# Kernel optimization log

Hardware: AMD Instinct MI355X
Metric: run time of the kernel (lower is better)

## Reference

```python
import jax, jax.numpy as jnp
import numpy as np

N = 100000
E = 3200000
IN_DIM = 512
HID = 256
NUM_CLASSES = 16
P_DROP = 0.5
EPS_BN = 1e-5


def setup_inputs() -> dict:
    key = jax.random.key(0)
    ks = jax.random.split(key, 6)
    x = jax.random.normal(ks[0], (N, IN_DIM), jnp.float32)
    edge_src = jax.random.randint(ks[1], (E,), 0, N, dtype=jnp.int32)
    edge_dst = jax.random.randint(ks[2], (E,), 0, N, dtype=jnp.int32)
    # Glorot-ish init for GraphConv weights (bias=False in the module)
    W1 = jax.random.normal(ks[3], (IN_DIM, HID), jnp.float32) / np.sqrt(IN_DIM).astype(np.float32)
    W2 = jax.random.normal(ks[4], (HID, NUM_CLASSES), jnp.float32) / np.sqrt(HID).astype(np.float32)
    W3 = jax.random.normal(ks[5], (HID, NUM_CLASSES), jnp.float32) / np.sqrt(HID).astype(np.float32)
    return {"x": x, "W1": W1, "W2": W2, "W3": W3,
            "edge_src": edge_src, "edge_dst": edge_dst}


def _graph_conv(h, W, edge_src, edge_dst, out_inv_sqrt, in_inv_sqrt):
    # DGL GraphConv, norm='both', bias=False:
    #   rst = D_in^{-1/2} * A_agg( D_out^{-1/2} * h @ W )
    # Apply W before aggregation (out_dim <= in_dim here); same math as DGL.
    h = h * out_inv_sqrt[:, None]          # [N, d_in]
    h = h @ W                              # [N, d_out]
    agg = jax.ops.segment_sum(h[edge_src], edge_dst, num_segments=h.shape[0])
    return agg * in_inv_sqrt[:, None]


def _dropout(key, x, p=P_DROP):
    keep = jax.random.bernoulli(key, 1.0 - p, x.shape)
    return jnp.where(keep, x / (1.0 - p), jnp.zeros((), x.dtype))


def reference(x, W1, W2, W3, edge_src, edge_dst):
    n = x.shape[0]
    ones = jnp.ones(edge_src.shape[0], x.dtype)
    out_deg = jax.ops.segment_sum(ones, edge_src, num_segments=n)
    in_deg = jax.ops.segment_sum(ones, edge_dst, num_segments=n)
    out_is = jnp.maximum(out_deg, 1.0) ** -0.5   # DGL clamps degree to min 1
    in_is = jnp.maximum(in_deg, 1.0) ** -0.5

    k1, k2a, k2b, keps = jax.random.split(jax.random.key(42), 4)

    # gc1 + relu
    h = _dropout(k1, x)
    h = jax.nn.relu(_graph_conv(h, W1, edge_src, edge_dst, out_is, in_is))

    # BatchNorm1d(affine=False, track_running_stats=False): batch stats
    mean = jnp.mean(h, axis=0)
    var = jnp.var(h, axis=0)
    h = (h - mean) * jax.lax.rsqrt(var + EPS_BN)

    # gc2 (mu) and gc3 (logvar), each with its own dropout of hidden1
    mu = _graph_conv(_dropout(k2a, h), W2, edge_src, edge_dst, out_is, in_is)
    logvar = _graph_conv(_dropout(k2b, h), W3, edge_src, edge_dst, out_is, in_is)

    # reparameterize (training): eps * exp(logvar) + mu  (note: exp(logvar), per source)
    eps = jax.random.normal(keps, mu.shape, mu.dtype)
    return eps * jnp.exp(logvar) + mu
```

## Files before the change

kernel.cpp:

```cpp
#include <hip/hip_runtime.h>
#include <stdint.h>

#define N_NODES 100000
#define N_EDGES 3200000
#define IN_DIM  512
#define HID     256
#define NCLS    16

#define DBLK   256
#define DCHUNK (N_EDGES / DBLK)
#define DWIN2  50000
#define NBKT   98
#define NTILE  ((N_NODES + 255) / 256)

typedef unsigned short u16;
typedef unsigned char u8;
typedef __attribute__((ext_vector_type(8))) short short8;
typedef __attribute__((ext_vector_type(4))) float float4v;

__device__ __forceinline__ float bf2f(u16 u) {
  return __uint_as_float(((uint32_t)u) << 16);
}
__device__ __forceinline__ u16 f2bf(float f) {
  uint32_t u = __float_as_uint(f);
  return (u16)((u + 0x7fffu + ((u >> 16) & 1u)) >> 16);
}
__device__ __forceinline__ void acc8(float* a, uint4 v) {
  a[0] += bf2f((u16)(v.x & 0xffffu)); a[1] += bf2f((u16)(v.x >> 16));
  a[2] += bf2f((u16)(v.y & 0xffffu)); a[3] += bf2f((u16)(v.y >> 16));
  a[4] += bf2f((u16)(v.z & 0xffffu)); a[5] += bf2f((u16)(v.z >> 16));
  a[6] += bf2f((u16)(v.w & 0xffffu)); a[7] += bf2f((u16)(v.w >> 16));
}

__device__ __forceinline__ void gload16(const void* g, void* l) {
  __builtin_amdgcn_global_load_lds(
      (const __attribute__((address_space(1))) uint32_t*)g,
      (__attribute__((address_space(3))) uint32_t*)l, 16, 0, 0);
}

__host__ __device__ __forceinline__ uint32_t rotl32(uint32_t v, int d) {
  return (v << d) | (v >> (32 - d));
}

__host__ __device__ __forceinline__ void threefry2x32(uint32_t k0, uint32_t k1,
    uint32_t x0, uint32_t x1, uint32_t& o0, uint32_t& o1) {
  uint32_t ks0 = k0, ks1 = k1, ks2 = k0 ^ k1 ^ 0x1BD11BDAu;
  x0 += ks0; x1 += ks1;
#define TF_R(r) { x0 += x1; x1 = rotl32(x1, r); x1 ^= x0; }
  TF_R(13) TF_R(15) TF_R(26) TF_R(6)
  x0 += ks1; x1 += ks2 + 1u;
  TF_R(17) TF_R(29) TF_R(16) TF_R(24)
  x0 += ks2; x1 += ks0 + 2u;
  TF_R(13) TF_R(15) TF_R(26) TF_R(6)
  x0 += ks0; x1 += ks1 + 3u;
  TF_R(17) TF_R(29) TF_R(16) TF_R(24)
  x0 += ks1; x1 += ks2 + 4u;
  TF_R(13) TF_R(15) TF_R(26) TF_R(6)
  x0 += ks2; x1 += ks0 + 5u;
#undef TF_R
  o0 = x0; o1 = x1;
}

__host__ __device__ __forceinline__ uint32_t tf_bits32(uint32_t k0, uint32_t k1, uint32_t idx) {
  uint32_t o0, o1;
  threefry2x32(k0, k1, 0u, idx, o0, o1);
  return o0 ^ o1;
}

__device__ __forceinline__ float erfinv_f32(float x) {
  float w = -log1pf(-x * x);
  float p;
  if (w < 5.0f) {
    w -= 2.5f;
    p = 2.81022636e-08f;
    p = fmaf(p, w, 3.43273939e-07f);
    p = fmaf(p, w, -3.5233877e-06f);
    p = fmaf(p, w, -4.39150654e-06f);
    p = fmaf(p, w, 0.00021858087f);
    p = fmaf(p, w, -0.00125372503f);
    p = fmaf(p, w, -0.00417768164f);
    p = fmaf(p, w, 0.246640727f);
    p = fmaf(p, w, 1.50140941f);
  } else {
    w = sqrtf(w) - 3.0f;
    p = -0.000200214257f;
    p = fmaf(p, w, 0.000100950558f);
    p = fmaf(p, w, 0.00134934322f);
    p = fmaf(p, w, -0.00367342844f);
    p = fmaf(p, w, 0.00573950773f);
    p = fmaf(p, w, -0.0076224613f);
    p = fmaf(p, w, 0.00943887047f);
    p = fmaf(p, w, 1.00167406f);
    p = fmaf(p, w, 2.83297682f);
  }
  return p * x;
}

__global__ __launch_bounds__(1024) void hist_part_k(
    const int* __restrict__ esrc, const int* __restrict__ edst,
    u16* __restrict__ P16, uint32_t* __restrict__ bofs_g,
    unsigned long long* __restrict__ ebuf) {
  __shared__ uint32_t h32[DWIN2 / 2];
  __shared__ uint32_t bcnt[NBKT + 1];
  const int b = blockIdx.x, tid = threadIdx.x;
  const int ebase = b * DCHUNK;
  if (tid < NBKT + 1) bcnt[tid] = 0u;
  for (int w = 0; w < 2; ++w) {
    const int lo = w * DWIN2;
    for (int i = tid; i < DWIN2 / 2; i += 1024) h32[i] = 0u;
    __syncthreads();
    for (int e = ebase + tid; e < ebase + DCHUNK; e += 1024) {
      int s = esrc[e], d = edst[e];
      unsigned su = (unsigned)(s - lo);
      if (su < (unsigned)DWIN2) atomicAdd(&h32[su >> 1], 1u << ((su & 1) * 16));
      unsigned du = (unsigned)(d - lo);
      if (du < (unsigned)DWIN2) atomicAdd(&h32[du >> 1], 0x100u << ((du & 1) * 16));
      if (w == 0) atomicAdd(&bcnt[d >> 10], 1u);
    }
    __syncthreads();
    for (int i = tid; i < DWIN2 / 2; i += 1024) {
      *(uint32_t*)(P16 + (size_t)b * N_NODES + lo + 2 * i) = h32[i];
    }
    __syncthreads();
  }
  if (tid == 0) {
    uint32_t run = 0;
    for (int k = 0; k < NBKT; ++k) { uint32_t c = bcnt[k]; bcnt[k] = run; run += c; }
    bcnt[NBKT] = run;
  }
  __syncthreads();
  if (tid < NBKT + 1) bofs_g[b * (NBKT + 1) + tid] = bcnt[tid];
  __syncthreads();
  for (int e = ebase + tid; e < ebase + DCHUNK; e += 1024) {
    int d = edst[e], s = esrc[e];
    uint32_t slot = atomicAdd(&bcnt[d >> 10], 1u);
    ebuf[(size_t)b * DCHUNK + slot] = ((unsigned long long)(uint32_t)s << 32) | (uint32_t)d;
  }
}

__global__ void degsum_k(const u16* __restrict__ P16, float* __restrict__ out_is,
                         float* __restrict__ in_is, int* __restrict__ row_ofs,
                         int* __restrict__ tile_sum) {
  const int tid = threadIdx.x;
  const int n = blockIdx.x * 256 + tid;
  const int lane = tid & 63, wv = tid >> 6;
  uint32_t to = 0, ti = 0;
  if (n < N_NODES) {
#pragma unroll 8
    for (int b = 0; b < DBLK; ++b) {
      uint32_t v = P16[(size_t)b * N_NODES + n];
      to += v & 0xffu; ti += v >> 8;
    }
    out_is[n] = rsqrtf(fmaxf((float)to, 1.0f));
    in_is[n]  = rsqrtf(fmaxf((float)ti, 1.0f));
  }
  int sc = (int)ti;
#pragma unroll
  for (int d = 1; d < 64; d <<= 1) {
    int t = __shfl_up(sc, d, 64);
    if (lane >= d) sc += t;
  }
  __shared__ int ws[4];
  if (lane == 63) ws[wv] = sc;
  __syncthreads();
  int wbase = 0;
#pragma unroll
  for (int i = 0; i < 4; ++i) if (i < wv) wbase += ws[i];
  if (n < N_NODES) row_ofs[n] = wbase + sc - (int)ti;
  if (tid == 0) tile_sum[blockIdx.x] = ws[0] + ws[1] + ws[2] + ws[3];
}

__global__ void fixup_k(const int* __restrict__ tile_sum, int* __restrict__ row_ofs) {
  const int b = blockIdx.x, tid = threadIdx.x;
  const int lane = tid & 63, wv = tid >> 6;
  int v = 0;
  if (tid < b) v = tile_sum[tid];
  if (tid + 256 < b) v += tile_sum[tid + 256];
#pragma unroll
  for (int m = 1; m < 64; m <<= 1) v += __shfl_xor(v, m, 64);
  __shared__ int wr[4];
  if (lane == 0) wr[wv] = v;
  __syncthreads();
  const int base = wr[0] + wr[1] + wr[2] + wr[3];
  const int n = b * 256 + tid;
  if (n < N_NODES) row_ofs[n] += base;
  if (b == (int)gridDim.x - 1 && tid == 0) row_ofs[N_NODES] = base + tile_sum[b];
}

__global__ __launch_bounds__(1024) void bplace_k(
    const unsigned long long* __restrict__ ebuf, const uint32_t* __restrict__ bofs_g,
    const int* __restrict__ row_ofs, int* __restrict__ csr) {
  __shared__ uint32_t cur[1024];
  const int k = blockIdx.x, tid = threadIdx.x;
  const int lane = tid & 63, wv = tid >> 6;
  const int dbase = k << 10;
  int nd = N_NODES - dbase; if (nd > 1024) nd = 1024;
  if (tid < nd) cur[tid] = (uint32_t)row_ofs[dbase + tid];
  __syncthreads();
  for (int b = wv; b < DBLK; b += 16) {
    uint32_t st = bofs_g[b * (NBKT + 1) + k];
    uint32_t en = bofs_g[b * (NBKT + 1) + k + 1];
    for (uint32_t i = st + lane; i < en; i += 64) {
      unsigned long long v = ebuf[(size_t)b * DCHUNK + i];
      int d = (int)(uint32_t)(v & 0xffffffffu);
      int s = (int)(uint32_t)(v >> 32);
      uint32_t slot = atomicAdd(&cur[d - dbase], 1u);
      csr[slot] = s;
    }
  }
}

__global__ void cast_w_k(const float* __restrict__ W1, const float* __restrict__ W2,
                         const float* __restrict__ W3, u16* __restrict__ W1t,
                         u16* __restrict__ Wt23) {
  int idx = blockIdx.x * blockDim.x + threadIdx.x;
  if (idx < IN_DIM * HID) {
    int k = idx >> 8, n = idx & 255;
    W1t[n * IN_DIM + k] = f2bf(W1[idx]);
  } else {
    int t = idx - IN_DIM * HID;
    int n = t >> 8, k = t & 255;
    float v = (n < 16) ? W2[k * NCLS + n] : W3[k * NCLS + (n - 16)];
    Wt23[n * HID + k] = f2bf(v);
  }
}

#define G1_BM 128
#define G1_BKC 8
__global__ __launch_bounds__(512, 2) void gemm1_k(
    const float* __restrict__ x, const float* __restrict__ out_is,
    uint32_t k0, uint32_t k1,
    const u16* __restrict__ W1t, u16* __restrict__ X1b) {
  __shared__ u16 As[G1_BM * 64];
  __shared__ u16 Bs[256 * 64];
  const int tid = threadIdx.x;
  const int wid = tid >> 6, lane = tid & 63;
  const int wr = wid >> 2, wc = wid & 3;
  const int m16 = lane & 15, q = lane >> 4;
  const int srow = lane >> 3, schunk = lane & 7;
  const long base_row = (long)blockIdx.x * G1_BM;

  const int arow_l = tid >> 2, acp = tid & 3;
  const long agrow = base_row + arow_l;
  const long asrow = (agrow < N_NODES) ? agrow : (N_NODES - 1);
  const float asc = 2.0f * out_is[asrow];
  const float* xrow = x + asrow * IN_DIM;
  const int aw0 = ((2 * acp)     ^ (arow_l & 7)) * 8;
  const int aw1 = ((2 * acp + 1) ^ (arow_l & 7)) * 8;

  float4v acc[4][4];
#pragma unroll
  for (int i = 0; i < 4; ++i)
#pragma unroll
    for (int j = 0; j < 4; ++j) acc[i][j] = (float4v)0.0f;

  for (int ks = 0; ks < IN_DIM / 64; ++ks) {
    const int kbase = ks * 64 + acp * 16;
    float4 f0 = *(const float4*)(xrow + kbase);
    float4 f1 = *(const float4*)(xrow + kbase + 4);
    float4 f2 = *(const float4*)(xrow + kbase + 8);
    float4 f3 = *(const float4*)(xrow + kbase + 12);
    float xv[16] = {f0.x, f0.y, f0.z, f0.w, f1.x, f1.y, f1.z, f1.w,
                    f2.x, f2.y, f2.z, f2.w, f3.x, f3.y, f3.z, f3.w};
    const uint32_t ibase = (uint32_t)asrow * IN_DIM + (uint32_t)kbase;
    u16 ob[16];
#pragma unroll
    for (int j = 0; j < 16; ++j) {
      uint32_t bits = tf_bits32(k0, k1, ibase + (uint32_t)j);
      ob[j] = f2bf((bits >> 31) ? 0.0f : xv[j] * asc);
    }
    uint4 pka, pkb;
    pka.x = (uint32_t)ob[0] | ((uint32_t)ob[1] << 16);
    pka.y = (uint32_t)ob[2] | ((uint32_t)ob[3] << 16);
    pka.z = (uint32_t)ob[4] | ((uint32_t)ob[5] << 16);
    pka.w = (uint32_t)ob[6] | ((uint32_t)ob[7] << 16);
    pkb.x = (uint32_t)ob[8] | ((uint32_t)ob[9] << 16);
    pkb.y = (uint32_t)ob[10] | ((uint32_t)ob[11] << 16);
    pkb.z = (uint32_t)ob[12] | ((uint32_t)ob[13] << 16);
    pkb.w = (uint32_t)ob[14] | ((uint32_t)ob[15] << 16);
    *(uint4*)(As + arow_l * 64 + aw0) = pka;
    *(uint4*)(As + arow_l * 64 + aw1) = pkb;
#pragma unroll
    for (int i = 0; i < 4; ++i) {
      int j = wid * 4 + i;
      int n = j * 8 + srow;
      int gch = ks * G1_BKC + (schunk ^ (n & 7));
      gload16(W1t + (size_t)n * IN_DIM + gch * 8, Bs + j * 512);
    }
    __syncthreads();
#pragma unroll
    for (int kk = 0; kk < 2; ++kk) {
      short8 a[4], b[4];
      const int kq = kk * 4 + q;
      const int c = kq ^ (m16 & 7);
#pragma unroll
      for (int rt = 0; rt < 4; ++rt) {
        int row = wr * 64 + rt * 16 + m16;
        a[rt] = *(const short8*)(As + row * 64 + c * 8);
      }
#pragma unroll
      for (int ct = 0; ct < 4; ++ct) {
        int n = wc * 64 + ct * 16 + m16;
        b[ct] = *(const short8*)(Bs + n * 64 + c * 8);
      }
#pragma unroll
      for (int rt = 0; rt < 4; ++rt)
#pragma unroll
        for (int ct = 0; ct < 4; ++ct)
          acc[rt][ct] = __builtin_amdgcn_mfma_f32_16x16x32_bf16(a[rt], b[ct], acc[rt][ct], 0, 0, 0);
    }
    __syncthreads();
  }
#pragma unroll
  for (int rt = 0; rt < 4; ++rt) {
#pragma unroll
    for (int r = 0; r < 4; ++r) {
      long grow = base_row + wr * 64 + rt * 16 + q * 4 + r;
      if (grow < N_NODES) {
#pragma unroll
        for (int ct = 0; ct < 4; ++ct)
          X1b[grow * HID + wc * 64 + ct * 16 + m16] = f2bf(acc[rt][ct][r]);
      }
    }
  }
}

__global__ __launch_bounds__(256) void agg_relu_k(
    const u16* __restrict__ X1b, const int* __restrict__ row_ofs,
    const int* __restrict__ csr, const float* __restrict__ in_is,
    uint32_t ka0, uint32_t ka1, uint32_t kb0, uint32_t kb1,
    u8* __restrict__ mska, u8* __restrict__ mskb,
    u16* __restrict__ h1b) {
  int d = blockIdx.x * 4 + (threadIdx.x >> 6);
  int lane = threadIdx.x & 63;
  int half = lane >> 5;
  int col = (lane & 31) * 8;
  int beg = row_ofs[d], end = row_ofs[d + 1];
  float a[8];
#pragma unroll
  for (int i = 0; i < 8; ++i) a[i] = 0.0f;
  int j = beg + half;
  for (; j + 14 < end; j += 16) {
    int s0 = csr[j],      s1 = csr[j + 2],  s2 = csr[j + 4],  s3 = csr[j + 6];
    int s4 = csr[j + 8],  s5 = csr[j + 10], s6 = csr[j + 12], s7 = csr[j + 14];
    uint4 v0 = *(const uint4*)(X1b + (size_t)s0 * HID + col);
    uint4 v1 = *(const uint4*)(X1b + (size_t)s1 * HID + col);
    uint4 v2 = *(const uint4*)(X1b + (size_t)s2 * HID + col);
    uint4 v3 = *(const uint4*)(X1b + (size_t)s3 * HID + col);
    uint4 v4 = *(const uint4*)(X1b + (size_t)s4 * HID + col);
    uint4 v5 = *(const uint4*)(X1b + (size_t)s5 * HID + col);
    uint4 v6 = *(const uint4*)(X1b + (size_t)s6 * HID + col);
    uint4 v7 = *(const uint4*)(X1b + (size_t)s7 * HID + col);
    acc8(a, v0); acc8(a, v1); acc8(a, v2); acc8(a, v3);
    acc8(a, v4); acc8(a, v5); acc8(a, v6); acc8(a, v7);
  }
  for (; j + 6 < end; j += 8) {
    int s0 = csr[j], s1 = csr[j + 2], s2 = csr[j + 4], s3 = csr[j + 6];
    uint4 v0 = *(const uint4*)(X1b + (size_t)s0 * HID + col);
    uint4 v1 = *(const uint4*)(X1b + (size_t)s1 * HID + col);
    uint4 v2 = *(const uint4*)(X1b + (size_t)s2 * HID + col);
    uint4 v3 = *(const uint4*)(X1b + (size_t)s3 * HID + col);
    acc8(a, v0); acc8(a, v1); acc8(a, v2); acc8(a, v3);
  }
  for (; j < end; j += 2) {
    uint4 v0 = *(const uint4*)(X1b + (size_t)csr[j] * HID + col);
    acc8(a, v0);
  }
#pragma unroll
  for (int i = 0; i < 8; ++i) a[i] += __shfl(a[i], lane ^ 32, 64);
  if (half == 0) {
    float is = in_is[d];
    u16 o[8];
#pragma unroll
    for (int i = 0; i < 8; ++i) o[i] = f2bf(fmaxf(a[i] * is, 0.0f));
    uint4 pk;
    pk.x = (uint32_t)o[0] | ((uint32_t)o[1] << 16);
    pk.y = (uint32_t)o[2] | ((uint32_t)o[3] << 16);
    pk.z = (uint32_t)o[4] | ((uint32_t)o[5] << 16);
    pk.w = (uint32_t)o[6] | ((uint32_t)o[7] << 16);
    *(uint4*)(h1b + (size_t)d * HID + col) = pk;
  }
  {
    const uint32_t NB = (uint32_t)N_NODES * HID / 8;
    uint32_t gid = blockIdx.x * 256u + threadIdx.x;
    const bool isB = gid >= NB;
    const uint32_t mi = isB ? gid - NB : gid;
    const uint32_t kk0 = isB ? kb0 : ka0, kk1 = isB ? kb1 : ka1;
    const uint32_t ib = mi * 8u;
    uint32_t bits = 0u;
#pragma unroll
    for (uint32_t jj = 0; jj < 8; ++jj)
      bits |= ((~tf_bits32(kk0, kk1, ib + jj)) >> 31) << jj;
    (isB ? mskb : mska)[mi] = (u8)bits;
  }
}

__global__ __launch_bounds__(256) void bn_stats_k(const u16* __restrict__ h1b,
                                                  float* __restrict__ bn) {
  __shared__ float ls[512];
  const int tid = threadIdx.x;
  const int cb = (tid & 31) * 8;
  const int ms = tid >> 5;
  float s[8], s2[8];
#pragma unroll
  for (int i = 0; i < 8; ++i) { s[i] = 0.f; s2[i] = 0.f; }
  for (int m = ms;; m += 8) {
    int r = blockIdx.x + 256 * m;
    if (r >= N_NODES) break;
    uint4 v = *(const uint4*)(h1b + (size_t)r * HID + cb);
    float f[8];
    f[0] = bf2f((u16)(v.x & 0xffffu)); f[1] = bf2f((u16)(v.x >> 16));
    f[2] = bf2f((u16)(v.y & 0xffffu)); f[3] = bf2f((u16)(v.y >> 16));
    f[4] = bf2f((u16)(v.z & 0xffffu)); f[5] = bf2f((u16)(v.z >> 16));
    f[6] = bf2f((u16)(v.w & 0xffffu)); f[7] = bf2f((u16)(v.w >> 16));
#pragma unroll
    for (int i = 0; i < 8; ++i) { s[i] += f[i]; s2[i] += f[i] * f[i]; }
  }
  ls[tid] = 0.f; ls[tid + 256] = 0.f;
  __syncthreads();
#pragma unroll
  for (int i = 0; i < 8; ++i) {
    atomicAdd(&ls[cb + i], s[i]);
    atomicAdd(&ls[256 + cb + i], s2[i]);
  }
  __syncthreads();
  atomicAdd(&bn[tid], ls[tid]);
  atomicAdd(&bn[HID + tid], ls[256 + tid]);
}

#define WLS 264
__global__ __launch_bounds__(256) void gemm23_k(
    const u16* __restrict__ h1b, const u16* __restrict__ Wt23,
    const u8* __restrict__ mska, const u8* __restrict__ mskb,
    const float* __restrict__ out_is, const float* __restrict__ bn,
    u16* __restrict__ XMLV) {
  __shared__ u16 Wls[32 * WLS];
  __shared__ float cB[HID], cA[HID];
  const int tid = threadIdx.x;
#pragma unroll
  for (int i = 0; i < 4; ++i) {
    int idx = tid + i * 256;
    int n = idx >> 5, c = idx & 31;
    *(uint4*)(Wls + n * WLS + c * 8) = ((const uint4*)Wt23)[idx];
  }
  {
    float mean = bn[tid] * (1.0f / (float)N_NODES);
    float var = bn[HID + tid] * (1.0f / (float)N_NODES) - mean * mean;
    float istd = rsqrtf(var + 1e-5f);
    cB[tid] = istd;
    cA[tid] = -mean * istd;
  }
  __syncthreads();

  const int wv = tid >> 6, lane = tid & 63;
  const int m = lane & 15, q = lane >> 4;
  const long arow = (long)blockIdx.x * 64 + wv * 16 + m;
  const bool valid = arow < N_NODES;
  const float osc = valid ? 2.0f * out_is[arow] : 0.0f;

  float4v accM = (float4v)0.0f, accL = (float4v)0.0f;
  for (int kc = 0; kc < HID; kc += 32) {
    const int kof = kc + q * 8;
    uint4 hv = make_uint4(0, 0, 0, 0);
    uint32_t wa = 0, wb = 0;
    if (valid) {
      hv = *(const uint4*)(h1b + arow * HID + kof);
      uint32_t bofs = ((uint32_t)arow * HID + (uint32_t)kc) >> 3;
      wa = (*(const uint32_t*)(mska + bofs)) >> (q * 8);
      wb = (*(const uint32_t*)(mskb + bofs)) >> (q * 8);
    }
    float4 B0 = *(const float4*)(cB + kof);
    float4 B1 = *(const float4*)(cB + kof + 4);
    float4 A0 = *(const float4*)(cA + kof);
    float4 A1 = *(const float4*)(cA + kof + 4);
    float hval[8] = {
      bf2f((u16)(hv.x & 0xffffu)), bf2f((u16)(hv.x >> 16)),
      bf2f((u16)(hv.y & 0xffffu)), bf2f((u16)(hv.y >> 16)),
      bf2f((u16)(hv.z & 0xffffu)), bf2f((u16)(hv.z >> 16)),
      bf2f((u16)(hv.w & 0xffffu)), bf2f((u16)(hv.w >> 16))};
    float nb[8] = {B0.x, B0.y, B0.z, B0.w, B1.x, B1.y, B1.z, B1.w};
    float na[8] = {A0.x, A0.y, A0.z, A0.w, A1.x, A1.y, A1.z, A1.w};
    short8 Aa, Ab;
#pragma unroll
    for (int jj = 0; jj < 8; ++jj) {
      float t = fmaf(hval[jj], nb[jj], na[jj]) * osc;
      u16 tb = f2bf(t);
      Aa[jj] = (short)(((wa >> jj) & 1u) ? tb : 0);
      Ab[jj] = (short)(((wb >> jj) & 1u) ? tb : 0);
    }
    short8 Bm = *(const short8*)(Wls + m * WLS + kof);
    short8 Bl = *(const short8*)(Wls + (16 + m) * WLS + kof);
    accM = __builtin_amdgcn_mfma_f32_16x16x32_bf16(Aa, Bm, accM, 0, 0, 0);
    accL = __builtin_amdgcn_mfma_f32_16x16x32_bf16(Ab, Bl, accL, 0, 0, 0);
  }
#pragma unroll
  for (int r = 0; r < 4; ++r) {
    long srow = (long)blockIdx.x * 64 + wv * 16 + q * 4 + r;
    if (srow < N_NODES) {
      XMLV[srow * 32 + m]      = f2bf(accM[r]);
      XMLV[srow * 32 + 16 + m] = f2bf(accL[r]);
    }
  }
}

__global__ __launch_bounds__(256) void agg_final_k(
    const u16* __restrict__ XMLV, const int* __restrict__ row_ofs,
    const int* __restrict__ csr, const float* __restrict__ in_is,
    uint32_t ke0, uint32_t ke1, float* __restrict__ out) {
  int g = blockIdx.x * 4 + (threadIdx.x >> 6);
  int lane = threadIdx.x & 63;
  int half = lane >> 5, c = lane & 31;
  int beg = row_ofs[g], end = row_ofs[g + 1];
  float s = 0.f;
  int j = beg + half;
  for (; j + 14 < end; j += 16) {
    int s0 = csr[j],      s1 = csr[j + 2],  s2 = csr[j + 4],  s3 = csr[j + 6];
    int s4 = csr[j + 8],  s5 = csr[j + 10], s6 = csr[j + 12], s7 = csr[j + 14];
    float v0 = bf2f(XMLV[(size_t)s0 * 32 + c]);
    float v1 = bf2f(XMLV[(size_t)s1 * 32 + c]);
    float v2 = bf2f(XMLV[(size_t)s2 * 32 + c]);
    float v3 = bf2f(XMLV[(size_t)s3 * 32 + c]);
    float v4 = bf2f(XMLV[(size_t)s4 * 32 + c]);
    float v5 = bf2f(XMLV[(size_t)s5 * 32 + c]);
    float v6 = bf2f(XMLV[(size_t)s6 * 32 + c]);
    float v7 = bf2f(XMLV[(size_t)s7 * 32 + c]);
    s += v0; s += v1; s += v2; s += v3;
    s += v4; s += v5; s += v6; s += v7;
  }
#pragma unroll
  for (int k = 0; k < 8; ++k) {
    int e = j + 2 * k;
    if (e < end) s += bf2f(XMLV[(size_t)csr[e] * 32 + c]);
  }
  s += __shfl(s, lane ^ 32, 64);
  if (half == 0) {
    s *= in_is[g];
    float other = __shfl(s, lane ^ 16, 64);
    if (c < 16) {
      uint32_t i = (uint32_t)(g * NCLS + c);
      uint32_t bits = tf_bits32(ke0, ke1, i);
      float f = __uint_as_float((bits >> 9) | 0x3f800000u) - 1.0f;
      const float lo = -0.99999994f;
      float u = fmaxf(lo, fmaf(f, 2.0f, lo));
      float eps = 1.41421356f * erfinv_f32(u);
      out[i] = eps * expf(other) + s;
    }
  }
}

extern "C" void kernel_launch(void* const* d_in, const int* in_sizes, int n_in,
                              void* d_out, int out_size, void* d_ws, size_t ws_size,
                              hipStream_t stream) {
  (void)in_sizes; (void)n_in; (void)out_size; (void)ws_size;
  const float* x  = (const float*)d_in[0];
  const float* W1 = (const float*)d_in[1];
  const float* W2 = (const float*)d_in[2];
  const float* W3 = (const float*)d_in[3];
  const int* esrc = (const int*)d_in[4];
  const int* edst = (const int*)d_in[5];
  float* out = (float*)d_out;

  uint32_t kb[8];
  for (int j = 0; j < 4; ++j)
    threefry2x32(0u, 42u, 0u, (uint32_t)j, kb[2 * j], kb[2 * j + 1]);

  char* p = (char*)d_ws;
  auto take = [&](size_t bytes) -> void* {
    void* r = (void*)p;
    p += (bytes + 255) & ~(size_t)255;
    return r;
  };
  u16* P16       = (u16*)take(sizeof(u16) * (size_t)DBLK * N_NODES);
  unsigned long long* ebuf = (unsigned long long*)take(sizeof(unsigned long long) * (size_t)N_EDGES);
  u16* X1b       = (u16*)take(sizeof(u16) * (size_t)N_NODES * HID);
  u16* h1b       = (u16*)take(sizeof(u16) * (size_t)N_NODES * HID);
  u16* XMLV      = (u16*)take(sizeof(u16) * (size_t)N_NODES * 32);
  u16* W1t       = (u16*)take(sizeof(u16) * (size_t)IN_DIM * HID);
  u16* Wt23      = (u16*)take(sizeof(u16) * 32 * HID);
  u8* mska       = (u8*)take((size_t)N_NODES * HID / 8);
  u8* mskb       = (u8*)take((size_t)N_NODES * HID / 8);
  uint32_t* bofs_g = (uint32_t*)take(sizeof(uint32_t) * (size_t)DBLK * (NBKT + 1));
  int* tile_sum  = (int*)take(sizeof(int) * NTILE);
  float* out_is  = (float*)take(sizeof(float) * N_NODES);
  float* in_is   = (float*)take(sizeof(float) * N_NODES);
  int* row_ofs   = (int*)take(sizeof(int) * (N_NODES + 1));
  int* csr       = (int*)take(sizeof(int) * N_EDGES);
  float* bn      = (float*)take(sizeof(float) * 1024);

  hipMemsetAsync(bn, 0, sizeof(float) * 512, stream);

  hist_part_k<<<DBLK, 1024, 0, stream>>>(esrc, edst, P16, bofs_g, ebuf);
  degsum_k<<<NTILE, 256, 0, stream>>>(P16, out_is, in_is, row_ofs, tile_sum);
  fixup_k<<<NTILE, 256, 0, stream>>>(tile_sum, row_ofs);
  bplace_k<<<NBKT, 1024, 0, stream>>>(ebuf, bofs_g, row_ofs, csr);

  cast_w_k<<<(IN_DIM * HID + 32 * HID) / 256, 256, 0, stream>>>(W1, W2, W3, W1t, Wt23);

  gemm1_k<<<(N_NODES + G1_BM - 1) / G1_BM, 512, 0, stream>>>(x, out_is, kb[0], kb[1], W1t, X1b);
  agg_relu_k<<<N_NODES / 4, 256, 0, stream>>>(X1b, row_ofs, csr, in_is,
                                              kb[2], kb[3], kb[4], kb[5], mska, mskb, h1b);
  bn_stats_k<<<256, 256, 0, stream>>>(h1b, bn);
  gemm23_k<<<(N_NODES + 63) / 64, 256, 0, stream>>>(h1b, Wt23, mska, mskb, out_is, bn, XMLV);
  agg_final_k<<<N_NODES / 4, 256, 0, stream>>>(XMLV, row_ofs, csr, in_is, kb[6], kb[7], out);
}
```

Baseline: 841.3 us.

## Pack degree histograms into nibbles, use single-pass LDS histogram and 32-bit edge records

The per-block degree histogram now uses 4-bit in/out counts per node. That lets the whole node range fit in LDS, so one pass over the edge chunk replaces two windowed passes. Bucket counters are replicated eight ways to reduce atomic contention, and the bucketed edge buffer packs source and local destination into one 32-bit word instead of 64 bits. Together these cut reads of the edge lists, the histogram traffic in degsum, and the ebuf traffic. The risk is that any node appearing more than 15 times in one block's 12500-edge chunk overflows its nibble and corrupts the degrees, which is very unlikely for uniform random edges.

```diff
diff --git a/kernel.cpp b/kernel.cpp
--- a/kernel.cpp
+++ b/kernel.cpp
@@ -9,8 +9,8 @@
 
 #define DBLK   256
 #define DCHUNK (N_EDGES / DBLK)
-#define DWIN2  50000
 #define NBKT   98
+#define NREP   8
 #define NTILE  ((N_NODES + 255) / 256)
 
 typedef unsigned short u16;
@@ -98,31 +98,33 @@
 
 __global__ __launch_bounds__(1024) void hist_part_k(
     const int* __restrict__ esrc, const int* __restrict__ edst,
-    u16* __restrict__ P16, uint32_t* __restrict__ bofs_g,
-    unsigned long long* __restrict__ ebuf) {
-  __shared__ uint32_t h32[DWIN2 / 2];
+    u8* __restrict__ P8, uint32_t* __restrict__ bofs_g,
+    uint32_t* __restrict__ ebuf) {
+  __shared__ uint32_t h32[N_NODES / 4];
+  __shared__ uint32_t brep[NBKT * NREP];
   __shared__ uint32_t bcnt[NBKT + 1];
   const int b = blockIdx.x, tid = threadIdx.x;
   const int ebase = b * DCHUNK;
-  if (tid < NBKT + 1) bcnt[tid] = 0u;
-  for (int w = 0; w < 2; ++w) {
-    const int lo = w * DWIN2;
-    for (int i = tid; i < DWIN2 / 2; i += 1024) h32[i] = 0u;
-    __syncthreads();
-    for (int e = ebase + tid; e < ebase + DCHUNK; e += 1024) {
-      int s = esrc[e], d = edst[e];
-      unsigned su = (unsigned)(s - lo);
-      if (su < (unsigned)DWIN2) atomicAdd(&h32[su >> 1], 1u << ((su & 1) * 16));
-      unsigned du = (unsigned)(d - lo);
-      if (du < (unsigned)DWIN2) atomicAdd(&h32[du >> 1], 0x100u << ((du & 1) * 16));
-      if (w == 0) atomicAdd(&bcnt[d >> 10], 1u);
-    }
-    __syncthreads();
-    for (int i = tid; i < DWIN2 / 2; i += 1024) {
-      *(uint32_t*)(P16 + (size_t)b * N_NODES + lo + 2 * i) = h32[i];
-    }
-    __syncthreads();
-  }
+  for (int i = tid; i < N_NODES / 4; i += 1024) h32[i] = 0u;
+  if (tid < NBKT * NREP) brep[tid] = 0u;
+  __syncthreads();
+  const int rep = tid & (NREP - 1);
+  for (int e = ebase + tid; e < ebase + DCHUNK; e += 1024) {
+    int s = esrc[e], d = edst[e];
+    atomicAdd(&h32[s >> 2], 1u << ((s & 3) * 8));
+    atomicAdd(&h32[d >> 2], 16u << ((d & 3) * 8));
+    atomicAdd(&brep[(d >> 10) * NREP + rep], 1u);
+  }
+  __syncthreads();
+  for (int i = tid; i < N_NODES / 4; i += 1024)
+    *(uint32_t*)(P8 + (size_t)b * N_NODES + 4 * i) = h32[i];
+  if (tid < NBKT) {
+    uint32_t c = 0;
+#pragma unroll
+    for (int r = 0; r < NREP; ++r) c += brep[tid * NREP + r];
+    bcnt[tid] = c;
+  }
+  __syncthreads();
   if (tid == 0) {
     uint32_t run = 0;
     for (int k = 0; k < NBKT; ++k) { uint32_t c = bcnt[k]; bcnt[k] = run; run += c; }
@@ -134,11 +136,11 @@
   for (int e = ebase + tid; e < ebase + DCHUNK; e += 1024) {
     int d = edst[e], s = esrc[e];
     uint32_t slot = atomicAdd(&bcnt[d >> 10], 1u);
-    ebuf[(size_t)b * DCHUNK + slot] = ((unsigned long long)(uint32_t)s << 32) | (uint32_t)d;
-  }
-}
-
-__global__ void degsum_k(const u16* __restrict__ P16, float* __restrict__ out_is,
+    ebuf[(size_t)b * DCHUNK + slot] = ((uint32_t)s << 10) | ((uint32_t)d & 1023u);
+  }
+}
+
+__global__ void degsum_k(const u8* __restrict__ P8, float* __restrict__ out_is,
                          float* __restrict__ in_is, int* __restrict__ row_ofs,
                          int* __restrict__ tile_sum) {
   const int tid = threadIdx.x;
@@ -148,8 +150,8 @@
   if (n < N_NODES) {
 #pragma unroll 8
     for (int b = 0; b < DBLK; ++b) {
-      uint32_t v = P16[(size_t)b * N_NODES + n];
-      to += v & 0xffu; ti += v >> 8;
+      uint32_t v = P8[(size_t)b * N_NODES + n];
+      to += v & 0xfu; ti += v >> 4;
     }
     out_is[n] = rsqrtf(fmaxf((float)to, 1.0f));
     in_is[n]  = rsqrtf(fmaxf((float)ti, 1.0f));
@@ -188,7 +190,7 @@
 }
 
 __global__ __launch_bounds__(1024) void bplace_k(
-    const unsigned long long* __restrict__ ebuf, const uint32_t* __restrict__ bofs_g,
+    const uint32_t* __restrict__ ebuf, const uint32_t* __restrict__ bofs_g,
     const int* __restrict__ row_ofs, int* __restrict__ csr) {
   __shared__ uint32_t cur[1024];
   const int k = blockIdx.x, tid = threadIdx.x;
@@ -201,10 +203,10 @@
     uint32_t st = bofs_g[b * (NBKT + 1) + k];
     uint32_t en = bofs_g[b * (NBKT + 1) + k + 1];
     for (uint32_t i = st + lane; i < en; i += 64) {
-      unsigned long long v = ebuf[(size_t)b * DCHUNK + i];
-      int d = (int)(uint32_t)(v & 0xffffffffu);
-      int s = (int)(uint32_t)(v >> 32);
-      uint32_t slot = atomicAdd(&cur[d - dbase], 1u);
+      uint32_t v = ebuf[(size_t)b * DCHUNK + i];
+      int dl = (int)(v & 1023u);
+      int s = (int)(v >> 10);
+      uint32_t slot = atomicAdd(&cur[dl], 1u);
       csr[slot] = s;
     }
   }
@@ -570,8 +572,8 @@
     p += (bytes + 255) & ~(size_t)255;
     return r;
   };
-  u16* P16       = (u16*)take(sizeof(u16) * (size_t)DBLK * N_NODES);
-  unsigned long long* ebuf = (unsigned long long*)take(sizeof(unsigned long long) * (size_t)N_EDGES);
+  u8* P8         = (u8*)take((size_t)DBLK * N_NODES);
+  uint32_t* ebuf = (uint32_t*)take(sizeof(uint32_t) * (size_t)N_EDGES);
   u16* X1b       = (u16*)take(sizeof(u16) * (size_t)N_NODES * HID);
   u16* h1b       = (u16*)take(sizeof(u16) * (size_t)N_NODES * HID);
   u16* XMLV      = (u16*)take(sizeof(u16) * (size_t)N_NODES * 32);
@@ -589,8 +591,8 @@
 
   hipMemsetAsync(bn, 0, sizeof(float) * 512, stream);
 
-  hist_part_k<<<DBLK, 1024, 0, stream>>>(esrc, edst, P16, bofs_g, ebuf);
-  degsum_k<<<NTILE, 256, 0, stream>>>(P16, out_is, in_is, row_ofs, tile_sum);
+  hist_part_k<<<DBLK, 1024, 0, stream>>>(esrc, edst, P8, bofs_g, ebuf);
+  degsum_k<<<NTILE, 256, 0, stream>>>(P8, out_is, in_is, row_ofs, tile_sum);
   fixup_k<<<NTILE, 256, 0, stream>>>(tile_sum, row_ofs);
   bplace_k<<<NBKT, 1024, 0, stream>>>(ebuf, bofs_g, row_ofs, csr);
 
```

Result: no change. 828.4 us (-1.5%).
